# Optimization experiments

Hardware: AMD Instinct MI355X
Metric: run time of the kernel (lower is better)

## Reference

```python
import jax, jax.numpy as jnp
import numpy as np

Q_P = 127.0
EPS_LN = 1e-5
EPS_CLAMP = 1e-5


def setup_inputs() -> dict:
    key = jax.random.key(0)
    k1, k2 = jax.random.split(key)
    B, T, C_in, C_out, K = 8, 4096, 1024, 1024, 3
    x = jax.random.normal(k1, (B, T, C_in), dtype=jnp.float32)
    ln_gamma = jnp.ones((C_in,), dtype=jnp.float32)
    ln_beta = jnp.zeros((C_in,), dtype=jnp.float32)
    W = jax.random.normal(k2, (C_out, C_in, K), dtype=jnp.float32) * 0.02
    return {"x": x, "ln_gamma": ln_gamma, "ln_beta": ln_beta, "W": W}


def _layer_norm(x, g, b):
    mu = jnp.mean(x, axis=-1, keepdims=True)
    var = jnp.mean(jnp.square(x - mu), axis=-1, keepdims=True)
    return (x - mu) * jax.lax.rsqrt(var + EPS_LN) * g + b


def _activation_quant(x):
    # per-(batch,channel) abs-max over time axis (last axis of [B,C,T])
    gamma = jnp.maximum(jnp.max(jnp.abs(x), axis=-1, keepdims=True), EPS_CLAMP)
    scale = Q_P / gamma
    x_scaled = x * scale
    x_rounded = jnp.clip(jnp.round(x_scaled), -Q_P, Q_P)
    x_quant = jax.lax.stop_gradient(x_rounded - x_scaled) + x_scaled
    return x_quant, scale


def _weight_quant(w):
    beta = jnp.maximum(jnp.mean(jnp.abs(w)), EPS_CLAMP)
    w_scaled = w / beta
    w_rounded = jnp.round(jnp.clip(w_scaled, -1.0, 1.0))
    w_quant = jax.lax.stop_gradient(w_rounded - w_scaled) + w_scaled
    return w_quant, beta


def reference(x, ln_gamma, ln_beta, W):
    # x: [B, T, C_in]
    x_norm = _layer_norm(x, ln_gamma, ln_beta)
    x_t = jnp.transpose(x_norm, (0, 2, 1))  # [B, C_in, T]
    x_q, scale_x = _activation_quant(x_t)   # scale_x: [B, C_in, 1]
    w_q, beta_w = _weight_quant(W)
    y_raw = jax.lax.conv_general_dilated(
        x_q, w_q,
        window_strides=(1,), padding=[(1, 1)],
        dimension_numbers=("NCH", "OIH", "NCH"))  # [B, C_out, T]
    y = y_raw * (beta_w / scale_x)  # broadcast [B,C_in,1] over [B,C_out,T] (C_in==C_out)
    return jnp.transpose(y, (0, 2, 1))  # [B, T, C_out]
```

## Files before the change

### kernel.cpp

```cpp
#include <hip/hip_runtime.h>

#define B_  8
#define T_  4096
#define C_  1024
#define TP  4098
#define NW  (1024 * 1024)

typedef int   i32x4 __attribute__((ext_vector_type(4)));
typedef float f32x4 __attribute__((ext_vector_type(4)));

#define GLOAD16(g, l)                                                        \
    __builtin_amdgcn_global_load_lds(                                        \
        (const __attribute__((address_space(1))) void*)(g),                  \
        (__attribute__((address_space(3))) void*)(l), 16, 0, 0)

__global__ __launch_bounds__(256) void prefix1_kernel(
    const float* __restrict__ x, const float* __restrict__ lng,
    const float* __restrict__ lnb, const float* __restrict__ W,
    float2* __restrict__ stats, float* __restrict__ gpart,
    float* __restrict__ wpart, signed char* __restrict__ xq8) {
    const int blk = blockIdx.x;
    const int tid = threadIdx.x;

    if (blk >= 2064) {
        const int wb = blk - 2064;
        size_t i0 = ((size_t)wb * 256 + tid) * 64;
        float s = 0.0f;
#pragma unroll
        for (int j = 0; j < 16; ++j) {
            float4 a = *(const float4*)(W + i0 + j * 4);
            s += fabsf(a.x) + fabsf(a.y) + fabsf(a.z) + fabsf(a.w);
        }
#pragma unroll
        for (int off = 32; off > 0; off >>= 1) s += __shfl_down(s, off, 64);
        __shared__ float ps[4];
        const int wave = tid >> 6, lane = tid & 63;
        if (lane == 0) ps[wave] = s;
        __syncthreads();
        if (tid == 0) wpart[wb] = (ps[0] + ps[1]) + (ps[2] + ps[3]);
        return;
    }
    if (blk >= 2048) {
        const int i = (blk - 2048) * 256 + tid;
        const int r16 = i >> 8;
        const int b = r16 >> 1, side = r16 & 1;
        *(int*)(xq8 + ((size_t)b * TP + (size_t)side * (TP - 1)) * C_
                + (i & 255) * 4) = 0;
        return;
    }

    const int w = tid >> 6, l = tid & 63;
    const int row0 = blk * 16;
    __shared__ unsigned lmax[1024];
#pragma unroll
    for (int k = 0; k < 4; ++k) lmax[tid + k * 256] = 0u;
    __syncthreads();

    const int c0 = l * 16;
    float gv[16], bv[16], m[16];
#pragma unroll
    for (int j = 0; j < 4; ++j) {
        *(float4*)&gv[j * 4] = *(const float4*)(lng + c0 + j * 4);
        *(float4*)&bv[j * 4] = *(const float4*)(lnb + c0 + j * 4);
    }
#pragma unroll
    for (int j = 0; j < 16; ++j) m[j] = 0.0f;

#pragma unroll 2
    for (int rr = 0; rr < 4; ++rr) {
        const int row = row0 + w * 4 + rr;
        const float* xr = x + (size_t)row * C_ + c0;
        float v[16];
#pragma unroll
        for (int j = 0; j < 4; ++j) *(float4*)&v[j * 4] = *(const float4*)(xr + j * 4);
        float s = 0.0f, s2 = 0.0f;
#pragma unroll
        for (int j = 0; j < 16; ++j) { s += v[j]; s2 += v[j] * v[j]; }
#pragma unroll
        for (int off = 1; off < 64; off <<= 1) {
            s  += __shfl_xor(s,  off, 64);
            s2 += __shfl_xor(s2, off, 64);
        }
        const float mu   = s * (1.0f / C_);
        const float var  = fmaxf(s2 * (1.0f / C_) - mu * mu, 0.0f);
        const float rstd = 1.0f / sqrtf(var + 1e-5f);
        if (l == 0) stats[row] = make_float2(mu, rstd);
#pragma unroll
        for (int j = 0; j < 16; ++j)
            m[j] = fmaxf(m[j], fabsf((v[j] - mu) * rstd * gv[j] + bv[j]));
    }
#pragma unroll
    for (int j = 0; j < 16; ++j) atomicMax(&lmax[c0 + j], __float_as_uint(m[j]));
    __syncthreads();
#pragma unroll
    for (int k = 0; k < 4; ++k) {
        const int c = tid + k * 256;
        gpart[(size_t)blk * 1024 + c] = __uint_as_float(lmax[c]);
    }
}

__global__ __launch_bounds__(256) void prefix2_kernel(
    const float* __restrict__ gpart, const float* __restrict__ wpart,
    float* __restrict__ gamma_x, double* __restrict__ wsum) {
    const int blk = blockIdx.x;
    const int tid = threadIdx.x;
    if (blk < 32) {
        const int c = (blk & 3) * 256 + tid;
        const int b = blk >> 2;
        const float* p = gpart + (size_t)b * 256 * 1024 + c;
        float m = 0.0f;
#pragma unroll 8
        for (int i = 0; i < 256; ++i) m = fmaxf(m, p[(size_t)i * 1024]);
        gamma_x[b * 1024 + c] = m;
        return;
    }
    double s = (tid < 192) ? (double)wpart[tid] : 0.0;
#pragma unroll
    for (int off = 32; off > 0; off >>= 1) s += __shfl_down(s, off, 64);
    __shared__ double ps[4];
    const int wave = tid >> 6, lane = tid & 63;
    if (lane == 0) ps[wave] = s;
    __syncthreads();
    if (tid == 0) *wsum = (ps[0] + ps[1]) + (ps[2] + ps[3]);
}

__device__ __forceinline__ signed char quant1s(float xv, float2 s, float g,
                                               float be, float sc) {
    float xn = (xv - s.x) * s.y * g + be;
    float r  = rintf(xn * sc);
    r = fminf(fmaxf(r, -127.0f), 127.0f);
    return (signed char)(int)r;
}

__global__ __launch_bounds__(256) void quant_kernel(
    const float* __restrict__ x, const float2* __restrict__ stats,
    const float* __restrict__ lng, const float* __restrict__ lnb,
    const float* __restrict__ gamma_x, signed char* __restrict__ xq8,
    const float* __restrict__ W, const double* __restrict__ wsum,
    signed char* __restrict__ wq8, float* __restrict__ beta_out) {
    const int blk = blockIdx.x;
    const int tid = threadIdx.x;

    if (blk >= 8192) {
        const int gid = (blk - 8192) * 256 + tid;
        const float beta = fmaxf((float)(*wsum * (1.0 / 3145728.0)), 1e-5f);
        if (gid == 0) *beta_out = beta;
        const float* wp = W + (size_t)gid * 3;
#pragma unroll
        for (int k = 0; k < 3; ++k) {
            float s  = wp[k] / beta;
            float r  = rintf(fminf(fmaxf(s, -1.0f), 1.0f));
            wq8[(size_t)k * NW + gid] = (signed char)(int)r;
        }
        return;
    }

    const int r0 = blk * 4;
    const int b = r0 >> 12;
    const int c = tid * 4;
    float4 gv = *(const float4*)(lng + c);
    float4 bv = *(const float4*)(lnb + c);
    float4 gm = *(const float4*)(gamma_x + b * C_ + c);
    float4 sc;
    sc.x = 127.0f / fmaxf(gm.x, 1e-5f);
    sc.y = 127.0f / fmaxf(gm.y, 1e-5f);
    sc.z = 127.0f / fmaxf(gm.z, 1e-5f);
    sc.w = 127.0f / fmaxf(gm.w, 1e-5f);
#pragma unroll
    for (int rr = 0; rr < 4; ++rr) {
        const int row = r0 + rr, t = row & 4095;
        const float2 s = stats[row];
        float4 xv = *(const float4*)(x + (size_t)row * C_ + c);
        char4 qv;
        qv.x = quant1s(xv.x, s, gv.x, bv.x, sc.x);
        qv.y = quant1s(xv.y, s, gv.y, bv.y, sc.y);
        qv.z = quant1s(xv.z, s, gv.z, bv.z, sc.z);
        qv.w = quant1s(xv.w, s, gv.w, bv.w, sc.w);
        *(char4*)(xq8 + ((size_t)b * TP + t + 1) * C_ + c) = qv;
    }
}

__global__ __launch_bounds__(512, 2) void gemm_kernel(
    const signed char* __restrict__ xq8,
    const signed char* __restrict__ wq8,
    const float* __restrict__ gamma_x,
    const float* __restrict__ beta_p,
    float* __restrict__ out) {
    __shared__ __align__(16) signed char sA8[4][16384];
    __shared__ __align__(16) signed char sB8[4][16384];

    const int tid = threadIdx.x;
    const int w   = tid >> 6;
    const int l   = tid & 63;
    const int q   = l >> 4;
    const int lr  = l & 15;
    const int g16  = (q ^ ((lr >> 1) & 3)) * 16;
    const int sg16 = ((l & 3) ^ ((l >> 3) & 3)) * 16;

    const int d  = blockIdx.x;
    const int gg = (d & 7) + ((d >> 5) << 3);
    const int nt = (d >> 3) & 3;
    const int b  = gg >> 4;
    const int t0 = (gg & 15) << 8;
    const int n0 = nt << 8;

    const int wm = (w >> 2) * 128;
    const int wn = (w & 3) * 64;

    const signed char* A0 = xq8 + (size_t)(b * TP + t0) * C_;
    const signed char* Bq = wq8 + (size_t)n0 * C_;

    i32x4 acc[8][4] = {};
    i32x4 af[4], bf[4];

#define RD_A8(MI, SL, MS)                                                         \
    af[MI] = *(const i32x4*)&sA8[SL][(wm + (MS) * 64 + (MI) * 16 + lr) * 64 + g16]
#define RD_B8(SL) do {                                                            \
        _Pragma("unroll")                                                         \
        for (int ni = 0; ni < 4; ++ni)                                            \
            bf[ni] = *(const i32x4*)&sB8[SL][(wn + ni * 16 + lr) * 64 + g16];     \
    } while (0)

#define STG_A8(SLOT, S) do {                                                      \
        signed char* dA = &sA8[SLOT][0];                                          \
        const signed char* gA = A0 + (size_t)(S) * 64;                            \
        GLOAD16(gA + (size_t)(w * 16 + (l >> 2)) * C_ + sg16,                     \
                dA + w * 1024);                                                   \
        GLOAD16(gA + (size_t)(w * 16 + (l >> 2) + 128) * C_ + sg16,               \
                dA + 8192 + w * 1024);                                            \
    } while (0)
#define STG_B8(SLOT, S) do {                                                      \
        signed char* dB = &sB8[SLOT][0];                                          \
        const signed char* gB = Bq + (size_t)((S) >> 4) * NW + ((S) & 15) * 64;   \
        GLOAD16(gB + (size_t)(w * 16 + (l >> 2)) * C_ + sg16,                     \
                dB + w * 1024);                                                   \
        GLOAD16(gB + (size_t)(w * 16 + (l >> 2) + 128) * C_ + sg16,               \
                dB + 8192 + w * 1024);                                            \
    } while (0)

#define VM4 asm volatile("s_waitcnt vmcnt(4)" ::: "memory")
#define VM0 asm volatile("s_waitcnt vmcnt(0)" ::: "memory")
#define VMX do {} while (0)

#define PH8(AM, DOAF, ASL, AMS, DOBF, BSL, STGC, VMC, BAR) do {                   \
        STGC;                                                                     \
        asm volatile("s_waitcnt lgkmcnt(0)" ::: "memory");                        \
        __builtin_amdgcn_sched_barrier(0);                                        \
        __builtin_amdgcn_s_setprio(1);                                            \
        _Pragma("unroll")                                                         \
        for (int mi = 0; mi < 4; ++mi) {                                          \
            _Pragma("unroll")                                                     \
            for (int ni = 0; ni < 4; ++ni)                                        \
                acc[(AM) * 4 + mi][ni] = __builtin_amdgcn_mfma_i32_16x16x64_i8(   \
                    af[mi], bf[ni], acc[(AM) * 4 + mi][ni], 0, 0, 0);             \
            if (DOAF) { RD_A8(mi, ASL, AMS); }                                    \
            __builtin_amdgcn_sched_barrier(0);                                    \
        }                                                                         \
        __builtin_amdgcn_s_setprio(0);                                            \
        if (DOBF) { RD_B8(BSL); }                                                 \
        VMC;                                                                      \
        if (BAR) { __builtin_amdgcn_s_barrier();                                  \
                   __builtin_amdgcn_sched_barrier(0); }                           \
    } while (0)

#define TILE8(C0, S, STG_ON, VM1C, AF1, BF1, BAR1) do {                           \
        PH8(0, 1, (C0), 1, 0, 0,                                                  \
            { if (STG_ON) { STG_A8(((C0) + 3) & 3, (S) + 3); } }, VMX, 1);        \
        PH8(1, AF1, ((C0) + 1) & 3, 0, BF1, ((C0) + 1) & 3,                       \
            { if (STG_ON) { STG_B8(((C0) + 3) & 3, (S) + 3); } }, VM1C, BAR1);    \
    } while (0)

    STG_A8(0, 0); STG_B8(0, 0);
    STG_A8(1, 1); STG_B8(1, 1);
    STG_A8(2, 2); STG_B8(2, 2);
    VM4;
    __builtin_amdgcn_s_barrier();
    __builtin_amdgcn_sched_barrier(0);
    RD_A8(0, 0, 0); RD_A8(1, 0, 0); RD_A8(2, 0, 0); RD_A8(3, 0, 0);
    RD_B8(0);

#pragma unroll 1
    for (int it = 0; it < 11; ++it) {
        const int s0 = it * 4;
        TILE8(0, s0 + 0, 1, VM4, 1, 1, 1);
        TILE8(1, s0 + 1, 1, VM4, 1, 1, 1);
        TILE8(2, s0 + 2, 1, VM4, 1, 1, 1);
        TILE8(3, s0 + 3, 1, VM4, 1, 1, 1);
    }
    TILE8(0, 44, 1, VM4, 1, 1, 1);
    TILE8(1, 45, 0, VM0, 1, 1, 1);
    TILE8(2, 46, 0, VMX, 1, 1, 1);
    TILE8(3, 47, 0, VMX, 0, 0, 0);

    const float beta = *beta_p;
#pragma unroll
    for (int ni = 0; ni < 4; ++ni) {
        const int o = n0 + wn + ni * 16 + lr;
        const float sc = beta * fmaxf(gamma_x[b * C_ + o], 1e-5f) * (1.0f / 127.0f);
#pragma unroll
        for (int mi = 0; mi < 8; ++mi) {
#pragma unroll
            for (int r = 0; r < 4; ++r) {
                const int t = t0 + wm + mi * 16 + q * 4 + r;
                out[(size_t)(b * T_ + t) * C_ + o] = (float)acc[mi][ni][r] * sc;
            }
        }
    }
#undef RD_A8
#undef RD_B8
#undef STG_A8
#undef STG_B8
#undef PH8
#undef TILE8
}

extern "C" void kernel_launch(void* const* d_in, const int* in_sizes, int n_in,
                              void* d_out, int out_size, void* d_ws, size_t ws_size,
                              hipStream_t stream) {
    const float* x   = (const float*)d_in[0];
    const float* lng = (const float*)d_in[1];
    const float* lnb = (const float*)d_in[2];
    const float* W   = (const float*)d_in[3];
    float* out = (float*)d_out;

    char* ws = (char*)d_ws;
    float2*      stats = (float2*)(ws + 0);
    float*       gamma = (float*) (ws + 262144);
    double*      wsum  = (double*)(ws + 294912);
    float*       beta  = (float*) (ws + 294920);
    signed char* wq8   = (signed char*)(ws + 294928);
    signed char* xq8   = (signed char*)(ws + 3440656);
    float*       gpart = out;
    float*       wpart = out + 4 * 1024 * 1024;

    prefix1_kernel<<<2256,  256, 0, stream>>>(x, lng, lnb, W, stats, gpart, wpart, xq8);
    prefix2_kernel<<<33,    256, 0, stream>>>(gpart, wpart, gamma, wsum);
    quant_kernel  <<<12288, 256, 0, stream>>>(x, stats, lng, lnb, gamma, xq8,
                                              W, wsum, wq8, beta);
    gemm_kernel   <<<dim3(512), 512, 0, stream>>>(xq8, wq8, gamma, beta, out);
}
```

Measured before the change: 422.3 us.

## Use 16 waves per GEMM block with 64x64 per-wave tiles

Doubles the GEMM block to 1024 threads and halves each wave's output tile from 128x64 to 64x64, keeping the 256x256 block tile. The staging, fragment-read and MFMA schedule is rewritten around a single phase per k-step. The goal is more waves per CU to hide LDS and global latency, and fewer accumulator registers per wave. In exchange, each A/B fragment read from LDS feeds fewer MFMAs. The launch-bounds hint requesting 4 blocks may also squeeze the register budget enough to cause spills.

Result: faster. 410.4 us (-2.8%).

```diff
diff --git a/kernel.cpp b/kernel.cpp
--- a/kernel.cpp
+++ b/kernel.cpp
@@ -180,7 +180,7 @@
     }
 }
 
-__global__ __launch_bounds__(512, 2) void gemm_kernel(
+__global__ __launch_bounds__(1024, 4) void gemm_kernel(
     const signed char* __restrict__ xq8,
     const signed char* __restrict__ wq8,
     const float* __restrict__ gamma_x,
@@ -204,93 +204,82 @@
     const int t0 = (gg & 15) << 8;
     const int n0 = nt << 8;
 
-    const int wm = (w >> 2) * 128;
+    const int wm = (w >> 2) * 64;
     const int wn = (w & 3) * 64;
 
     const signed char* A0 = xq8 + (size_t)(b * TP + t0) * C_;
     const signed char* Bq = wq8 + (size_t)n0 * C_;
 
-    i32x4 acc[8][4] = {};
+    i32x4 acc[4][4] = {};
     i32x4 af[4], bf[4];
 
-#define RD_A8(MI, SL, MS)                                                         \
-    af[MI] = *(const i32x4*)&sA8[SL][(wm + (MS) * 64 + (MI) * 16 + lr) * 64 + g16]
-#define RD_B8(SL) do {                                                            \
-        _Pragma("unroll")                                                         \
-        for (int ni = 0; ni < 4; ++ni)                                            \
-            bf[ni] = *(const i32x4*)&sB8[SL][(wn + ni * 16 + lr) * 64 + g16];     \
-    } while (0)
-
-#define STG_A8(SLOT, S) do {                                                      \
-        signed char* dA = &sA8[SLOT][0];                                          \
-        const signed char* gA = A0 + (size_t)(S) * 64;                            \
-        GLOAD16(gA + (size_t)(w * 16 + (l >> 2)) * C_ + sg16,                     \
-                dA + w * 1024);                                                   \
-        GLOAD16(gA + (size_t)(w * 16 + (l >> 2) + 128) * C_ + sg16,               \
-                dA + 8192 + w * 1024);                                            \
-    } while (0)
-#define STG_B8(SLOT, S) do {                                                      \
-        signed char* dB = &sB8[SLOT][0];                                          \
-        const signed char* gB = Bq + (size_t)((S) >> 4) * NW + ((S) & 15) * 64;   \
-        GLOAD16(gB + (size_t)(w * 16 + (l >> 2)) * C_ + sg16,                     \
-                dB + w * 1024);                                                   \
-        GLOAD16(gB + (size_t)(w * 16 + (l >> 2) + 128) * C_ + sg16,               \
-                dB + 8192 + w * 1024);                                            \
-    } while (0)
-
-#define VM4 asm volatile("s_waitcnt vmcnt(4)" ::: "memory")
+#define RD_A8(MI, SL)                                                             \
+    af[MI] = *(const i32x4*)&sA8[SL][(wm + (MI) * 16 + lr) * 64 + g16]
+#define RD_B8(NI, SL)                                                             \
+    bf[NI] = *(const i32x4*)&sB8[SL][(wn + (NI) * 16 + lr) * 64 + g16]
+
+#define STG_A8(SLOT, S)                                                           \
+    GLOAD16(A0 + (size_t)(S) * 64 + (size_t)(w * 16 + (l >> 2)) * C_ + sg16,      \
+            &sA8[SLOT][0] + w * 1024)
+#define STG_B8(SLOT, S)                                                           \
+    GLOAD16(Bq + (size_t)((S) >> 4) * NW + ((S) & 15) * 64                        \
+            + (size_t)(w * 16 + (l >> 2)) * C_ + sg16,                            \
+            &sB8[SLOT][0] + w * 1024)
+
+#define VM2 asm volatile("s_waitcnt vmcnt(2)" ::: "memory")
 #define VM0 asm volatile("s_waitcnt vmcnt(0)" ::: "memory")
 #define VMX do {} while (0)
-
-#define PH8(AM, DOAF, ASL, AMS, DOBF, BSL, STGC, VMC, BAR) do {                   \
-        STGC;                                                                     \
+#define SB  __builtin_amdgcn_sched_barrier(0)
+
+#define MFMA8(MI, NI)                                                             \
+    acc[MI][NI] = __builtin_amdgcn_mfma_i32_16x16x64_i8(                          \
+        af[MI], bf[NI], acc[MI][NI], 0, 0, 0)
+
+#define GRP(MI) do {                                                              \
+        _Pragma("unroll")                                                         \
+        for (int ni = 0; ni < 4; ++ni) MFMA8(MI, ni);                             \
+    } while (0)
+
+#define TILE(C0, S, STG_ON, VMC, DONXT, BAR) do {                                 \
+        const int nsl = ((C0) + 1) & 3;                                           \
+        if (STG_ON) { STG_A8(((C0) + 3) & 3, (S) + 3);                            \
+                      STG_B8(((C0) + 3) & 3, (S) + 3); }                          \
         asm volatile("s_waitcnt lgkmcnt(0)" ::: "memory");                        \
-        __builtin_amdgcn_sched_barrier(0);                                        \
+        SB;                                                                       \
         __builtin_amdgcn_s_setprio(1);                                            \
-        _Pragma("unroll")                                                         \
-        for (int mi = 0; mi < 4; ++mi) {                                          \
-            _Pragma("unroll")                                                     \
-            for (int ni = 0; ni < 4; ++ni)                                        \
-                acc[(AM) * 4 + mi][ni] = __builtin_amdgcn_mfma_i32_16x16x64_i8(   \
-                    af[mi], bf[ni], acc[(AM) * 4 + mi][ni], 0, 0, 0);             \
-            if (DOAF) { RD_A8(mi, ASL, AMS); }                                    \
-            __builtin_amdgcn_sched_barrier(0);                                    \
-        }                                                                         \
+        GRP(0); if (DONXT) { RD_A8(0, nsl); } SB;                                 \
+        GRP(1); if (DONXT) { RD_A8(1, nsl); } SB;                                 \
+        GRP(2); if (DONXT) { RD_A8(2, nsl); } SB;                                 \
+        MFMA8(3, 0); if (DONXT) { RD_B8(0, nsl); } SB;                            \
+        MFMA8(3, 1); if (DONXT) { RD_B8(1, nsl); } SB;                            \
+        MFMA8(3, 2); if (DONXT) { RD_B8(2, nsl); } SB;                            \
+        MFMA8(3, 3); if (DONXT) { RD_B8(3, nsl); RD_A8(3, nsl); } SB;             \
         __builtin_amdgcn_s_setprio(0);                                            \
-        if (DOBF) { RD_B8(BSL); }                                                 \
         VMC;                                                                      \
-        if (BAR) { __builtin_amdgcn_s_barrier();                                  \
-                   __builtin_amdgcn_sched_barrier(0); }                           \
-    } while (0)
-
-#define TILE8(C0, S, STG_ON, VM1C, AF1, BF1, BAR1) do {                           \
-        PH8(0, 1, (C0), 1, 0, 0,                                                  \
-            { if (STG_ON) { STG_A8(((C0) + 3) & 3, (S) + 3); } }, VMX, 1);        \
-        PH8(1, AF1, ((C0) + 1) & 3, 0, BF1, ((C0) + 1) & 3,                       \
-            { if (STG_ON) { STG_B8(((C0) + 3) & 3, (S) + 3); } }, VM1C, BAR1);    \
+        if (BAR) { __builtin_amdgcn_s_barrier(); SB; }                            \
     } while (0)
 
     STG_A8(0, 0); STG_B8(0, 0);
     STG_A8(1, 1); STG_B8(1, 1);
     STG_A8(2, 2); STG_B8(2, 2);
-    VM4;
+    VM2;
     __builtin_amdgcn_s_barrier();
-    __builtin_amdgcn_sched_barrier(0);
-    RD_A8(0, 0, 0); RD_A8(1, 0, 0); RD_A8(2, 0, 0); RD_A8(3, 0, 0);
-    RD_B8(0);
+    SB;
+    RD_A8(0, 0); RD_A8(1, 0); RD_A8(2, 0); RD_A8(3, 0);
+    RD_B8(0, 0); RD_B8(1, 0); RD_B8(2, 0); RD_B8(3, 0);
 
 #pragma unroll 1
     for (int it = 0; it < 11; ++it) {
         const int s0 = it * 4;
-        TILE8(0, s0 + 0, 1, VM4, 1, 1, 1);
-        TILE8(1, s0 + 1, 1, VM4, 1, 1, 1);
-        TILE8(2, s0 + 2, 1, VM4, 1, 1, 1);
-        TILE8(3, s0 + 3, 1, VM4, 1, 1, 1);
-    }
-    TILE8(0, 44, 1, VM4, 1, 1, 1);
-    TILE8(1, 45, 0, VM0, 1, 1, 1);
-    TILE8(2, 46, 0, VMX, 1, 1, 1);
-    TILE8(3, 47, 0, VMX, 0, 0, 0);
+        TILE(0, s0 + 0, 1, VM2, 1, 1);
+        TILE(1, s0 + 1, 1, VM2, 1, 1);
+        TILE(2, s0 + 2, 1, VM2, 1, 1);
+        TILE(3, s0 + 3, 1, VM2, 1, 1);
+    }
+    TILE(0, 44, 1, VM2, 1, 1);
+    TILE(1, 45, 0, VM0, 1, 1);
+    TILE(2, 46, 0, VMX, 1, 1);
+    TILE(3, 47, 0, VMX, 0, 0);
 
     const float beta = *beta_p;
 #pragma unroll
@@ -298,7 +287,7 @@
         const int o = n0 + wn + ni * 16 + lr;
         const float sc = beta * fmaxf(gamma_x[b * C_ + o], 1e-5f) * (1.0f / 127.0f);
 #pragma unroll
-        for (int mi = 0; mi < 8; ++mi) {
+        for (int mi = 0; mi < 4; ++mi) {
 #pragma unroll
             for (int r = 0; r < 4; ++r) {
                 const int t = t0 + wm + mi * 16 + q * 4 + r;
@@ -310,8 +299,9 @@
 #undef RD_B8
 #undef STG_A8
 #undef STG_B8
-#undef PH8
-#undef TILE8
+#undef MFMA8
+#undef GRP
+#undef TILE
 }
 
 extern "C" void kernel_launch(void* const* d_in, const int* in_sizes, int n_in,
@@ -337,5 +327,5 @@
     prefix2_kernel<<<33,    256, 0, stream>>>(gpart, wpart, gamma, wsum);
     quant_kernel  <<<12288, 256, 0, stream>>>(x, stats, lng, lnb, gamma, xq8,
                                               W, wsum, wq8, beta);
-    gemm_kernel   <<<dim3(512), 512, 0, stream>>>(xq8, wq8, gamma, beta, out);
-}
+    gemm_kernel   <<<dim3(512), 1024, 0, stream>>>(xq8, wq8, gamma, beta, out);
+}
```
